# Kernel optimization log

Hardware: AMD Instinct MI355X
Metric: run time of the kernel (lower is better)

## Reference

```python
import jax, jax.numpy as jnp
import numpy as np
from jax import lax

B, N, C = 8, 16384, 81          # batch, rois, total_labels
MAX_TOTAL = 100                  # max_total_size == max_output_size_per_class
IOU_THR = 0.5
VARIANCES = (0.1, 0.1, 0.2, 0.2)
NEG = -1e30                      # sentinel for suppressed/invalid slots


def setup_inputs() -> dict:
    key = jax.random.key(0)
    k1, k2, k3 = jax.random.split(key, 3)
    # roi boxes in [0,1]; sort corner pairs so y1<=y2, x1<=x2 (valid boxes)
    pts = jax.random.uniform(k1, (B, N, 2, 2), dtype=jnp.float32)
    lo = pts.min(axis=2)
    hi = pts.max(axis=2)
    roi = jnp.stack([lo[..., 0], lo[..., 1], hi[..., 0], hi[..., 1]], axis=-1)
    deltas = jax.random.normal(k2, (B, N, C * 4), dtype=jnp.float32)
    probs = jax.random.uniform(k3, (B, N, C), dtype=jnp.float32)
    return {"roi_bboxes": roi, "pred_deltas": deltas, "pred_label_probs": probs}


def _bboxes_from_deltas(anchors, deltas):
    # anchors: (..., 4) [y1,x1,y2,x2]; deltas: (..., 4) [dy,dx,dh,dw]
    aw = anchors[..., 3] - anchors[..., 1]
    ah = anchors[..., 2] - anchors[..., 0]
    acx = anchors[..., 1] + 0.5 * aw
    acy = anchors[..., 0] + 0.5 * ah
    bw = jnp.exp(deltas[..., 3]) * aw
    bh = jnp.exp(deltas[..., 2]) * ah
    bcx = deltas[..., 1] * aw + acx
    bcy = deltas[..., 0] * ah + acy
    y1 = bcy - 0.5 * bh
    x1 = bcx - 0.5 * bw
    y2 = bh + y1
    x2 = bw + x1
    return jnp.stack([y1, x1, y2, x2], axis=-1)


def _nms_keep(boxes):
    # boxes: (K, 4). Greedy NMS, returns bool keep mask of shape (K,).
    y1, x1, y2, x2 = boxes[..., 0], boxes[..., 1], boxes[..., 2], boxes[..., 3]
    area = (y2 - y1) * (x2 - x1)
    iy1 = jnp.maximum(y1[:, None], y1[None, :])
    ix1 = jnp.maximum(x1[:, None], x1[None, :])
    iy2 = jnp.minimum(y2[:, None], y2[None, :])
    ix2 = jnp.minimum(x2[:, None], x2[None, :])
    inter = jnp.clip(iy2 - iy1, 0.0) * jnp.clip(ix2 - ix1, 0.0)
    union = area[:, None] + area[None, :] - inter
    iou = inter / jnp.maximum(union, 1e-12)
    K = boxes.shape[0]
    idx = jnp.arange(K)

    def body(i, keep):
        suppress = keep[i] & (iou[i] > IOU_THR) & (idx > i)
        return keep & ~suppress

    return lax.fori_loop(0, K, body, jnp.ones((K,), dtype=bool))


def _forward(roi_bboxes, pred_deltas, pred_label_probs):
    b, n, _ = roi_bboxes.shape
    var = jnp.asarray(VARIANCES, dtype=pred_deltas.dtype)
    deltas = pred_deltas.reshape(b, n, C, 4) * var  # (B,N,C,4)
    anchors = roi_bboxes[:, :, None, :]             # broadcast over classes
    boxes = jnp.clip(_bboxes_from_deltas(anchors, deltas), 0.0, 1.0)  # (B,N,C,4)

    # zero scores where argmax class is background (class 0)
    labels_map = jnp.argmax(pred_label_probs, axis=-1, keepdims=True)  # (B,N,1)
    scores = jnp.where(labels_map != 0, pred_label_probs, 0.0)         # (B,N,C)

    # per-class top-K candidates (score_threshold is -inf in the original call)
    K = MAX_TOTAL
    scores_t = jnp.swapaxes(scores, 1, 2)              # (B,C,N)
    top_scores, top_idx = lax.top_k(scores_t, K)       # (B,C,K)
    boxes_t = jnp.swapaxes(boxes, 1, 2)                # (B,C,N,4)
    top_boxes = jnp.take_along_axis(boxes_t, top_idx[..., None], axis=2)  # (B,C,K,4)

    # greedy NMS per (batch, class); keep mask is index-like (non-diff)
    keep = jax.vmap(jax.vmap(_nms_keep))(lax.stop_gradient(top_boxes))  # (B,C,K)

    classes = jnp.broadcast_to(
        jnp.arange(C, dtype=jnp.float32)[None, :, None], (b, C, K))

    keyed = jnp.where(keep, top_scores, NEG).reshape(b, C * K)
    boxes_f = top_boxes.reshape(b, C * K, 4)
    scores_f = top_scores.reshape(b, C * K)
    classes_f = classes.reshape(b, C * K)

    sel_key, sel_idx = lax.top_k(keyed, MAX_TOTAL)                 # (B,100)
    sel_boxes = jnp.take_along_axis(boxes_f, sel_idx[..., None], axis=1)
    sel_scores = jnp.take_along_axis(scores_f, sel_idx, axis=1)
    sel_classes = jnp.take_along_axis(classes_f, sel_idx, axis=1)

    valid = sel_key > (NEG * 0.5)                                  # kept entries
    out_boxes = jnp.where(valid[..., None], sel_boxes, 0.0)
    out_classes = jnp.where(valid, sel_classes, 0.0)
    out_scores = jnp.where(valid, sel_scores, 0.0)
    return out_boxes, out_classes, out_scores


def reference(roi_bboxes, pred_deltas, pred_label_probs):
    return _forward(roi_bboxes, pred_deltas, pred_label_probs)
```

## Files before the change

kernel.cpp:

```cpp
#include <hip/hip_runtime.h>

#define B_ 8
#define N_ 16384
#define C_ 81
#define K_ 100
#define M_ (C_ * K_)
#define NEG_ (-1e30f)
#define IOU_THR_ 0.5f
#define TAU0_ 0.96f
#define TAU_ 0.985f
#define CHUNK_ 128
#define NCHUNK_ (N_ / CHUNK_)
#define CAPC_ 16
#define CAP_ 768
#define KCAP_ 256

__device__ inline unsigned key_of(float v) {
  unsigned u = __float_as_uint(v);
  return u ^ ((unsigned)((int)u >> 31) | 0x80000000u);
}

__device__ inline void find_kth_bin(unsigned* hist, unsigned* scan, unsigned kth,
                                    unsigned* out_b, unsigned* out_g) {
  int tid = threadIdx.x;
  int base = tid << 4;
  unsigned local = 0;
#pragma unroll
  for (int i = 0; i < 16; ++i) local += hist[base + ((tid + i) & 15)];
  scan[tid] = local;
  __syncthreads();
  for (int off = 1; off < 256; off <<= 1) {
    unsigned add = (tid + off < 256) ? scan[tid + off] : 0u;
    __syncthreads();
    scan[tid] += add;
    __syncthreads();
  }
  unsigned inclusive = scan[tid];
  unsigned after = inclusive - local;
  if (after < kth && inclusive >= kth) {
    unsigned g = after;
    for (int b = 15; b >= 0; --b) {
      unsigned c = hist[base + b];
      if (g + c >= kth) { *out_b = (unsigned)(base + b); *out_g = g; break; }
      g += c;
    }
  }
  __syncthreads();
}

__global__ __launch_bounds__(256) void kFused(const float* __restrict__ probs,
                                              unsigned long long* __restrict__ bgm,
                                              unsigned* __restrict__ pcnt,
                                              float* __restrict__ cand_val,
                                              int* __restrict__ cand_idx) {
  int gid = blockIdx.x;
  int b = gid >> 7;
  int q = gid & (NCHUNK_ - 1);
  int tid = threadIdx.x;

  __shared__ float tile[CHUNK_ * C_];
  __shared__ float lval[C_][CAPC_];
  __shared__ int   lidx[C_][CAPC_];
  __shared__ unsigned lcnt[C_];
  __shared__ unsigned char bgb[CHUNK_];

  const float4* src4 = (const float4*)(probs + ((size_t)b * N_ + (size_t)q * CHUNK_) * C_);
  float4* tile4 = (float4*)tile;
  for (int i = tid; i < (CHUNK_ * C_) / 4; i += 256) tile4[i] = src4[i];
  if (tid < C_) lcnt[tid] = 0;
  __syncthreads();

  int r = tid >> 1;
  int half = tid & 1;
  const float* row = &tile[r * C_];
  float p0 = row[0];
  int j0 = 1 + half * 40;
  float hm = -1.0f;
  for (int j = j0; j < j0 + 40; ++j) hm = fmaxf(hm, row[j]);
  float mx = fmaxf(hm, __shfl_xor(hm, 1));
  bool bg = (p0 >= mx);
  if (half == 0) bgb[r] = bg ? 1 : 0;
  if (!bg) {
    int n = q * CHUNK_ + r;
    if (half == 0 && p0 > TAU0_) {
      unsigned s = atomicAdd(&lcnt[0], 1u);
      if (s < CAPC_) { lval[0][s] = p0; lidx[0][s] = n; }
    }
    for (int j = j0; j < j0 + 40; ++j) {
      float v = row[j];
      if (v > TAU_) {
        unsigned s = atomicAdd(&lcnt[j], 1u);
        if (s < CAPC_) { lval[j][s] = v; lidx[j][s] = n; }
      }
    }
  }
  __syncthreads();

  if (tid < CHUNK_) {
    unsigned long long bal = __ballot(bgb[tid] != 0);
    if ((tid & 63) == 0)
      bgm[(((size_t)b * N_ + (size_t)q * CHUNK_) >> 6) + (tid >> 6)] = bal;
  }
  if (tid < C_) {
    unsigned lc = lcnt[tid];
    unsigned wr = lc < CAPC_ ? lc : CAPC_;
    size_t seg = ((size_t)(b * C_ + tid) * NCHUNK_ + q);
    pcnt[seg] = lc;
    float* dv = cand_val + seg * CAPC_;
    int*   di = cand_idx + seg * CAPC_;
    for (unsigned s = 0; s < wr; ++s) { dv[s] = lval[tid][s]; di[s] = lidx[tid][s]; }
  }
}

__global__ __launch_bounds__(256) void k_sel(const float* __restrict__ probs,
                                             const unsigned long long* __restrict__ bgm,
                                             const unsigned* __restrict__ pcnt,
                                             const float* __restrict__ cand_val,
                                             const int* __restrict__ cand_idx,
                                             const float* __restrict__ roi,
                                             const float* __restrict__ deltas,
                                             float* __restrict__ top_sc,
                                             float* __restrict__ top_box,
                                             int* __restrict__ keep_out) {
  int bc = blockIdx.x;
  int b = bc / C_, c = bc % C_;
  int tid = threadIdx.x;
  __shared__ float cv[CAP_];
  __shared__ int   ci[CAP_];
  __shared__ unsigned spc[NCHUNK_];
  __shared__ int     spre[NCHUNK_ + 1];
  __shared__ int     s_total;
  __shared__ int     s_ovf;
  __shared__ float selv[K_];
  __shared__ int   seli[K_];
  __shared__ float bx0[K_], bx1[K_], bx2[K_], bx3[K_], bar[K_];
  __shared__ unsigned chosen[N_ / 32];
  __shared__ float rv[4];
  __shared__ int   ri[4];

  if (tid == 0) s_ovf = 0;
  for (int t = tid; t < NCHUNK_; t += 256) {
    unsigned lc = pcnt[(size_t)bc * NCHUNK_ + t];
    spc[t] = lc;
    if (lc > CAPC_) atomicOr(&s_ovf, 1);
  }
  __syncthreads();
  if (tid == 0) {
    int acc = 0;
    for (int qq = 0; qq < NCHUNK_; ++qq) {
      spre[qq] = acc;
      unsigned lc = spc[qq];
      acc += (int)(lc < CAPC_ ? lc : CAPC_);
    }
    spre[NCHUNK_] = acc;
    s_total = acc;
  }
  __syncthreads();
  int total = s_total;
  bool fast = (!s_ovf && total >= K_ && total <= CAP_);

  if (fast) {
    for (int t = tid; t < NCHUNK_ * CAPC_; t += 256) {
      int qq = t >> 4, s = t & (CAPC_ - 1);
      if ((unsigned)s < spc[qq]) {
        size_t seg = (size_t)bc * NCHUNK_ + qq;
        int pos = spre[qq] + s;
        cv[pos] = cand_val[seg * CAPC_ + s];
        ci[pos] = cand_idx[seg * CAPC_ + s];
      }
    }
    __syncthreads();
    for (int t = tid; t < total; t += 256) {
      float mv = cv[t];
      int   mi = ci[t];
      int rank = 0;
      for (int j = 0; j < total; ++j) {
        float v = cv[j]; int ji = ci[j];
        rank += (v > mv || (v == mv && ji < mi)) ? 1 : 0;
      }
      if (rank < K_) { selv[rank] = mv; seli[rank] = mi; }
    }
    __syncthreads();
  } else {
    for (int i = tid; i < N_ / 32; i += 256) chosen[i] = 0u;
    __syncthreads();
    for (int k = 0; k < K_; ++k) {
      float bv = -1.0f;
      int   bi = 0;
      for (int n = tid; n < N_; n += 256) {
        if ((chosen[n >> 5] >> (n & 31)) & 1u) continue;
        unsigned long long w = bgm[((size_t)b * N_ + n) >> 6];
        float v = ((w >> (n & 63)) & 1ull) ? 0.0f
                 : probs[((size_t)b * N_ + n) * C_ + c];
        if (v > bv || (v == bv && n < bi)) { bv = v; bi = n; }
      }
      int lane = tid & 63, wave = tid >> 6;
      for (int off = 32; off > 0; off >>= 1) {
        float ov = __shfl_down(bv, off);
        int   oi = __shfl_down(bi, off);
        if (ov > bv || (ov == bv && oi < bi)) { bv = ov; bi = oi; }
      }
      if (lane == 0) { rv[wave] = bv; ri[wave] = bi; }
      __syncthreads();
      if (tid == 0) {
        float fv = rv[0]; int fi = ri[0];
        for (int w2 = 1; w2 < 4; ++w2)
          if (rv[w2] > fv || (rv[w2] == fv && ri[w2] < fi)) { fv = rv[w2]; fi = ri[w2]; }
        selv[k] = fv; seli[k] = fi;
        chosen[fi >> 5] |= (1u << (fi & 31));
      }
      __syncthreads();
    }
  }

  if (tid < K_) {
    int n = seli[tid];
    float4 a = *(const float4*)(roi + ((size_t)b * N_ + n) * 4);
    float4 d = *(const float4*)(deltas + ((size_t)b * N_ + n) * (C_ * 4) + (c << 2));
    float aw = a.w - a.y, ah = a.z - a.x;
    float acx = a.y + 0.5f * aw, acy = a.x + 0.5f * ah;
    float d0 = d.x * 0.1f, d1 = d.y * 0.1f, d2 = d.z * 0.2f, d3 = d.w * 0.2f;
    float bw = expf(d3) * aw, bh = expf(d2) * ah;
    float bcx = d1 * aw + acx, bcy = d0 * ah + acy;
    float y1 = bcy - 0.5f * bh, x1 = bcx - 0.5f * bw;
    float y2 = bh + y1, x2 = bw + x1;
    y1 = fminf(fmaxf(y1, 0.0f), 1.0f);
    x1 = fminf(fmaxf(x1, 0.0f), 1.0f);
    y2 = fminf(fmaxf(y2, 0.0f), 1.0f);
    x2 = fminf(fmaxf(x2, 0.0f), 1.0f);
    bx0[tid] = y1; bx1[tid] = x1; bx2[tid] = y2; bx3[tid] = x2;
    bar[tid] = (y2 - y1) * (x2 - x1);
    top_sc[bc * K_ + tid] = selv[tid];
    *(float4*)(top_box + ((size_t)bc * K_ + tid) * 4) = make_float4(y1, x1, y2, x2);
  }
  __syncthreads();

  if (tid < 64) {
    float Ay1 = bx0[tid], Ax1 = bx1[tid], Ay2 = bx2[tid], Ax2 = bx3[tid], Aar = bar[tid];
    int hasB = (tid + 64 < K_);
    float By1 = 0, Bxx1 = 0, By2 = 0, Bxx2 = 0, Bar2 = 0;
    if (hasB) { By1 = bx0[tid+64]; Bxx1 = bx1[tid+64]; By2 = bx2[tid+64]; Bxx2 = bx3[tid+64]; Bar2 = bar[tid+64]; }
    int ka = 1, kb = hasB;
    for (int i = 0; i < K_; ++i) {
      int src = i & 63;
      bool hi = (i >= 64);
      float iy1 = __shfl(hi ? By1 : Ay1, src);
      float ix1 = __shfl(hi ? Bxx1 : Ax1, src);
      float iy2 = __shfl(hi ? By2 : Ay2, src);
      float ix2 = __shfl(hi ? Bxx2 : Ax2, src);
      float iar = __shfl(hi ? Bar2 : Aar, src);
      int   ki  = __shfl(hi ? kb : ka, src);
      if (ki) {
        if (ka && tid > i) {
          float yy1 = fmaxf(iy1, Ay1), xx1 = fmaxf(ix1, Ax1);
          float yy2 = fminf(iy2, Ay2), xx2 = fminf(ix2, Ax2);
          float inter = fmaxf(yy2 - yy1, 0.0f) * fmaxf(xx2 - xx1, 0.0f);
          float uni = iar + Aar - inter;
          if (inter / fmaxf(uni, 1e-12f) > IOU_THR_) ka = 0;
        }
        if (kb && (tid + 64) > i) {
          float yy1 = fmaxf(iy1, By1), xx1 = fmaxf(ix1, Bxx1);
          float yy2 = fminf(iy2, By2), xx2 = fminf(ix2, Bxx2);
          float inter = fmaxf(yy2 - yy1, 0.0f) * fmaxf(xx2 - xx1, 0.0f);
          float uni = iar + Bar2 - inter;
          if (inter / fmaxf(uni, 1e-12f) > IOU_THR_) kb = 0;
        }
      }
    }
    keep_out[bc * K_ + tid] = ka;
    if (hasB) keep_out[bc * K_ + tid + 64] = kb;
  }
}

__global__ __launch_bounds__(256) void k4_final(const float* __restrict__ top_sc,
                                                const float* __restrict__ top_box,
                                                const int* __restrict__ keep_in,
                                                float* __restrict__ out) {
  int b = blockIdx.x;
  int tid = threadIdx.x;
  __shared__ float keyed[M_];
  __shared__ unsigned hist[4096];
  __shared__ unsigned scan[256];
  __shared__ unsigned s_b1, s_g1, s_b2, s_g2, s_cnt;
  __shared__ float cv[KCAP_];
  __shared__ int   ci[KCAP_];
  __shared__ int   sel_m[K_];
  __shared__ float sel_v[K_];

  for (int m = tid; m < M_; m += 256)
    keyed[m] = keep_in[b * M_ + m] ? top_sc[b * M_ + m] : NEG_;
  for (int i = tid; i < 4096; i += 256) hist[i] = 0;
  if (tid == 0) s_cnt = 0;
  __syncthreads();
  for (int m = tid; m < M_; m += 256) atomicAdd(&hist[key_of(keyed[m]) >> 20], 1u);
  __syncthreads();
  find_kth_bin(hist, scan, K_, &s_b1, &s_g1);
  unsigned b1 = s_b1;
  unsigned need1 = K_ - s_g1;
  __syncthreads();
  for (int i = tid; i < 4096; i += 256) hist[i] = 0;
  __syncthreads();
  for (int m = tid; m < M_; m += 256) {
    unsigned k = key_of(keyed[m]);
    if ((k >> 20) == b1) atomicAdd(&hist[(k >> 8) & 0xFFFu], 1u);
  }
  __syncthreads();
  find_kth_bin(hist, scan, need1, &s_b2, &s_g2);
  unsigned t24 = (b1 << 12) | s_b2;
  __syncthreads();
  for (int m = tid; m < M_; m += 256) {
    float v = keyed[m];
    unsigned k = key_of(v);
    if ((k >> 8) >= t24) {
      unsigned p = atomicAdd(&s_cnt, 1u);
      if (p < KCAP_) { cv[p] = v; ci[p] = m; }
    }
  }
  __syncthreads();
  int cnt = (int)min(s_cnt, (unsigned)KCAP_);
  if (tid < cnt) {
    float mv = cv[tid];
    int   mi = ci[tid];
    int rank = 0;
    for (int j = 0; j < cnt; ++j) {
      float v = cv[j]; int ji = ci[j];
      rank += (v > mv || (v == mv && ji < mi)) ? 1 : 0;
    }
    if (rank < K_) { sel_m[rank] = mi; sel_v[rank] = mv; }
  }
  __syncthreads();

  float* ob = out;
  float* oc = out + B_ * K_ * 4;
  float* os = oc + B_ * K_;
  if (tid < K_) {
    int m = sel_m[tid];
    float kv = sel_v[tid];
    bool valid = kv > (NEG_ * 0.5f);
    float4 bb = *(const float4*)(top_box + ((size_t)b * M_ + m) * 4);
    float sv = top_sc[b * M_ + m];
    float cls = (float)(m / K_);
    float4 o = valid ? bb : make_float4(0.f, 0.f, 0.f, 0.f);
    *(float4*)(ob + ((size_t)b * K_ + tid) * 4) = o;
    oc[b * K_ + tid] = valid ? cls : 0.0f;
    os[b * K_ + tid] = valid ? sv : 0.0f;
  }
}

extern "C" void kernel_launch(void* const* d_in, const int* in_sizes, int n_in,
                              void* d_out, int out_size, void* d_ws, size_t ws_size,
                              hipStream_t stream) {
  const float* roi    = (const float*)d_in[0];
  const float* deltas = (const float*)d_in[1];
  const float* probs  = (const float*)d_in[2];
  float* out = (float*)d_out;

  char* ws = (char*)d_ws;
  size_t off = 0;
  unsigned long long* bgm = (unsigned long long*)(ws + off);
  off += (size_t)B_ * N_ / 64 * sizeof(unsigned long long);
  unsigned* pcnt = (unsigned*)(ws + off);
  off += (size_t)B_ * C_ * NCHUNK_ * sizeof(unsigned);
  float* cand_val = (float*)(ws + off);
  off += (size_t)B_ * C_ * NCHUNK_ * CAPC_ * sizeof(float);
  int* cand_idx = (int*)(ws + off);
  off += (size_t)B_ * C_ * NCHUNK_ * CAPC_ * sizeof(int);
  float* top_sc = (float*)(ws + off);  off += (size_t)B_ * M_ * sizeof(float);
  float* top_box = (float*)(ws + off); off += (size_t)B_ * M_ * 4 * sizeof(float);
  int* keepA = (int*)(ws + off);       off += (size_t)B_ * M_ * sizeof(int);
  (void)ws_size; (void)in_sizes; (void)n_in; (void)out_size;

  kFused<<<B_ * NCHUNK_, 256, 0, stream>>>(probs, bgm, pcnt, cand_val, cand_idx);
  k_sel<<<B_ * C_, 256, 0, stream>>>(probs, bgm, pcnt, cand_val, cand_idx,
                                     roi, deltas, top_sc, top_box, keepA);
  k4_final<<<B_, 256, 0, stream>>>(top_sc, top_box, keepA, out);
}
```

Baseline: 118.6 us.

## Halve scan chunk to 64 rows, four threads per row, parallel prefix scan

Shrinks the per-block row chunk from 128 to 64, so twice as many blocks run the first kernel, and each row is split across four threads instead of two. The selection kernel now has 256 chunks per (batch,class), so its serial prefix sum over chunk counts becomes a block-wide Hillis-Steele scan with one thread per chunk. The aim is more parallelism and a shorter per-row loop in the scan kernel. The cost is twice as many per-chunk count and candidate segments to write and read in the selection kernel.

```diff
diff --git a/kernel.cpp b/kernel.cpp
--- a/kernel.cpp
+++ b/kernel.cpp
@@ -9,7 +9,7 @@
 #define IOU_THR_ 0.5f
 #define TAU0_ 0.96f
 #define TAU_ 0.985f
-#define CHUNK_ 128
+#define CHUNK_ 64
 #define NCHUNK_ (N_ / CHUNK_)
 #define CAPC_ 16
 #define CAP_ 768
@@ -54,7 +54,7 @@
                                               float* __restrict__ cand_val,
                                               int* __restrict__ cand_idx) {
   int gid = blockIdx.x;
-  int b = gid >> 7;
+  int b = gid >> 8;
   int q = gid & (NCHUNK_ - 1);
   int tid = threadIdx.x;
 
@@ -70,23 +70,25 @@
   if (tid < C_) lcnt[tid] = 0;
   __syncthreads();
 
-  int r = tid >> 1;
-  int half = tid & 1;
+  int r = tid >> 2;
+  int t = tid & 3;
+  int lane = tid & 63;
   const float* row = &tile[r * C_];
+  int j0 = 1 + t * 20;
+  float hm = -1.0f;
+  for (int j = j0; j < j0 + 20; ++j) hm = fmaxf(hm, row[j]);
+  hm = fmaxf(hm, __shfl_xor(hm, 1));
+  hm = fmaxf(hm, __shfl_xor(hm, 2));
   float p0 = row[0];
-  int j0 = 1 + half * 40;
-  float hm = -1.0f;
-  for (int j = j0; j < j0 + 40; ++j) hm = fmaxf(hm, row[j]);
-  float mx = fmaxf(hm, __shfl_xor(hm, 1));
-  bool bg = (p0 >= mx);
-  if (half == 0) bgb[r] = bg ? 1 : 0;
+  bool bg = (p0 >= hm);
+  if (t == 0) bgb[r] = bg ? 1 : 0;
   if (!bg) {
     int n = q * CHUNK_ + r;
-    if (half == 0 && p0 > TAU0_) {
+    if (t == 0 && p0 > TAU0_) {
       unsigned s = atomicAdd(&lcnt[0], 1u);
       if (s < CAPC_) { lval[0][s] = p0; lidx[0][s] = n; }
     }
-    for (int j = j0; j < j0 + 40; ++j) {
+    for (int j = j0; j < j0 + 20; ++j) {
       float v = row[j];
       if (v > TAU_) {
         unsigned s = atomicAdd(&lcnt[j], 1u);
@@ -98,8 +100,7 @@
 
   if (tid < CHUNK_) {
     unsigned long long bal = __ballot(bgb[tid] != 0);
-    if ((tid & 63) == 0)
-      bgm[(((size_t)b * N_ + (size_t)q * CHUNK_) >> 6) + (tid >> 6)] = bal;
+    if (lane == 0) bgm[(size_t)b * NCHUNK_ + q] = bal;
   }
   if (tid < C_) {
     unsigned lc = lcnt[tid];
@@ -128,7 +129,8 @@
   __shared__ float cv[CAP_];
   __shared__ int   ci[CAP_];
   __shared__ unsigned spc[NCHUNK_];
-  __shared__ int     spre[NCHUNK_ + 1];
+  __shared__ int     sscan[NCHUNK_];
+  __shared__ int     spre[NCHUNK_];
   __shared__ int     s_total;
   __shared__ int     s_ovf;
   __shared__ float selv[K_];
@@ -139,21 +141,21 @@
   __shared__ int   ri[4];
 
   if (tid == 0) s_ovf = 0;
-  for (int t = tid; t < NCHUNK_; t += 256) {
-    unsigned lc = pcnt[(size_t)bc * NCHUNK_ + t];
-    spc[t] = lc;
+  {
+    unsigned lc = pcnt[(size_t)bc * NCHUNK_ + tid];
+    spc[tid] = lc;
     if (lc > CAPC_) atomicOr(&s_ovf, 1);
-  }
-  __syncthreads();
-  if (tid == 0) {
-    int acc = 0;
-    for (int qq = 0; qq < NCHUNK_; ++qq) {
-      spre[qq] = acc;
-      unsigned lc = spc[qq];
-      acc += (int)(lc < CAPC_ ? lc : CAPC_);
-    }
-    spre[NCHUNK_] = acc;
-    s_total = acc;
+    int own = (int)(lc < CAPC_ ? lc : CAPC_);
+    sscan[tid] = own;
+    __syncthreads();
+    for (int off = 1; off < 256; off <<= 1) {
+      int add = (tid >= off) ? sscan[tid - off] : 0;
+      __syncthreads();
+      sscan[tid] += add;
+      __syncthreads();
+    }
+    spre[tid] = sscan[tid] - own;
+    if (tid == 255) s_total = sscan[255];
   }
   __syncthreads();
   int total = s_total;
@@ -358,7 +360,7 @@
   char* ws = (char*)d_ws;
   size_t off = 0;
   unsigned long long* bgm = (unsigned long long*)(ws + off);
-  off += (size_t)B_ * N_ / 64 * sizeof(unsigned long long);
+  off += (size_t)B_ * NCHUNK_ * sizeof(unsigned long long);
   unsigned* pcnt = (unsigned*)(ws + off);
   off += (size_t)B_ * C_ * NCHUNK_ * sizeof(unsigned);
   float* cand_val = (float*)(ws + off);
```

Measured after the change: 117.3 us. No clear change (-1.1%).
